# Kernel optimization log

Hardware: AMD Instinct MI355X
Metric: run time of the kernel (lower is better)

Reference implementation:

```python
import jax, jax.numpy as jnp
import numpy as np
import itertools

B, K, H, W = 64, 5, 320, 320
EPS = 1e-6
# All K! permutations (exact equivalent of scipy.linear_sum_assignment for KxK cost)
PERMS = np.array(list(itertools.permutations(range(K))), dtype=np.int32)  # [P, K]


def setup_inputs() -> dict:
    key = jax.random.key(0)
    k1, k2, k3 = jax.random.split(key, 3)
    return {
        "fg_logits": jax.random.normal(k1, (B, 1, H, W), dtype=jnp.float32),
        "slot_logits": jax.random.normal(k2, (B, K, H, W), dtype=jnp.float32),
        "target": jax.random.uniform(k3, (B, 1, H, W), dtype=jnp.float32),
    }


def reference(fg_logits, slot_logits, target):
    fg = target[:, 0]            # [B,H,W]
    bg = 1.0 - fg                # [B,H,W]
    # targets_b: index 0 = FG mask, 1..K-1 = BG mask (duplicated)  -> [B,K,H,W]
    targets = jnp.concatenate([fg[:, None], jnp.broadcast_to(bg[:, None], (B, K - 1, H, W))], axis=1)

    # IoU cost matrix on detached sigmoid probs (matches .detach())
    probs = jax.lax.stop_gradient(jax.nn.sigmoid(slot_logits))
    s = probs.reshape(B, K, -1)        # [B,K,N]
    t = targets.reshape(B, K, -1)      # [B,K,N]
    inter = jnp.einsum('bkn,bjn->bkj', s, t)           # [B,K,K]
    union = s.sum(-1)[:, :, None] + t.sum(-1)[:, None, :] - inter + EPS
    cost = 1.0 - inter / union                          # [B,K,K]

    # Exact Hungarian via brute force over K! permutations (K small)
    perms = jnp.asarray(PERMS)                          # [P,K]
    rows = jnp.arange(K)[None, :]                       # [1,K]
    perm_cost = cost[:, rows, perms].sum(-1)            # [B,P]
    best_perm = perms[jnp.argmin(perm_cost, axis=1)]    # [B,K] col_ind per sample

    # aligned[i] = targets[col_ind[i]]; targets[j] is fg iff j == 0
    is_fg = (best_perm == 0)[:, :, None, None]          # [B,K,1,1]
    aligned = jnp.where(is_fg, fg[:, None], bg[:, None])  # [B,K,H,W]

    # Stable sigmoid-BCE with logits, mean-reduced per sample then averaged over B
    x = slot_logits
    bce = jnp.maximum(x, 0.0) - x * aligned + jnp.log1p(jnp.exp(-jnp.abs(x)))
    return bce.mean()
```

## Files before the change

### kernel.cpp

```cpp
#include <hip/hip_runtime.h>


#define BB 64
#define KK 5
#define NPIX 102400
#define Q 50
#define SEG (NPIX / Q)
#define THREADS 256
#define ITERS (SEG / (THREADS * 4))
#define REC 32
#define NVAL 26
#define NBLK (BB * Q)

typedef float f4 __attribute__((ext_vector_type(4)));

__global__ void hung_pass1(const float* __restrict__ slot,
                           const float* __restrict__ tgt,
                           float* __restrict__ ws)
{
    const int bid = blockIdx.x;
    const int b   = bid / Q;
    const int q   = bid - b * Q;

    const float* sb = slot + (size_t)b * KK * NPIX + q * SEG;
    const float* t  = tgt  + (size_t)b * NPIX      + q * SEG;

    float aX[KK]  = {0,0,0,0,0};
    float aXF[KK] = {0,0,0,0,0};
    float aS[KK]  = {0,0,0,0,0};
    float aSF[KK] = {0,0,0,0,0};
    float aPX[KK] = {0,0,0,0,0};
    float Tf = 0.f;

    const int base = threadIdx.x * 4;
    #pragma unroll
    for (int i = 0; i < ITERS; ++i) {
        const int off = base + i * (THREADS * 4);
        const f4 fg4 = *reinterpret_cast<const f4*>(t + off);
        f4 x4[KK];
        #pragma unroll
        for (int k = 0; k < KK; ++k)
            x4[k] = *reinterpret_cast<const f4*>(sb + (size_t)k * NPIX + off);

        Tf += (fg4.x + fg4.y) + (fg4.z + fg4.w);

        #pragma unroll
        for (int k = 0; k < KK; ++k) {
            #pragma unroll
            for (int j = 0; j < 4; ++j) {
                const float x  = x4[k][j];
                const float fg = fg4[j];
                const float e  = __expf(-fabsf(x));
                const float L  = __logf(1.0f + e);
                const float d  = L + fmaxf(-x, 0.0f);
                const float s  = __expf(-d);
                aPX[k] += d;
                aX[k]  += x;
                aXF[k]  = fmaf(x, fg, aXF[k]);
                aS[k]  += s;
                aSF[k]  = fmaf(s, fg, aSF[k]);
            }
        }
    }

    float v[NVAL];
    #pragma unroll
    for (int k = 0; k < KK; ++k) {
        v[k*5+0] = aX[k];  v[k*5+1] = aXF[k]; v[k*5+2] = aS[k];
        v[k*5+3] = aSF[k]; v[k*5+4] = aPX[k];
    }
    v[25] = Tf;

    #pragma unroll
    for (int jv = 0; jv < NVAL; ++jv) {
        float x = v[jv];
        #pragma unroll
        for (int off = 32; off > 0; off >>= 1) x += __shfl_down(x, off, 64);
        v[jv] = x;
    }
    __shared__ float red[THREADS / 64][NVAL];
    const int lane = threadIdx.x & 63;
    const int w    = threadIdx.x >> 6;
    if (lane == 0) {
        #pragma unroll
        for (int jv = 0; jv < NVAL; ++jv) red[w][jv] = v[jv];
    }
    __syncthreads();
    if (threadIdx.x < NVAL) {
        const int jv = threadIdx.x;
        ws[(size_t)bid * REC + jv] =
            red[0][jv] + red[1][jv] + red[2][jv] + red[3][jv];
    }
}

__global__ __launch_bounds__(320) void hung_pass2(const float* __restrict__ ws,
                                                  float* __restrict__ out)
{
    __shared__ float red[BB][KK][6];
    const int t = threadIdx.x;
    {
        const int b = t / KK, k = t - (t / KK) * KK;
        float v[5] = {0, 0, 0, 0, 0};
        float tf = 0.f;
        for (int q = 0; q < Q; ++q) {
            const float* p = ws + (size_t)(b * Q + q) * REC;
            #pragma unroll
            for (int c = 0; c < 5; ++c) v[c] += p[k * 5 + c];
            if (k == 0) tf += p[25];
        }
        #pragma unroll
        for (int c = 0; c < 5; ++c) red[b][k][c] = v[c];
        if (k == 0) red[b][0][5] = tf;
    }
    __syncthreads();
    if (t < BB) {
        const int b = t;
        const float Tf = red[b][0][5];
        const float Tb = (float)NPIX - Tf;
        float best = 3.402823466e+38f; int kb = 0;
        float xfsum = 0.f, px = 0.f;
        #pragma unroll
        for (int k = 0; k < KK; ++k) {
            const float Sv = red[b][k][2], Iv = red[b][k][3];
            const float cf = 1.f - Iv / (Sv + Tf - Iv + 1e-6f);
            const float Ib = Sv - Iv;
            const float cb = 1.f - Ib / (Sv + Tb - Ib + 1e-6f);
            const float dd = cf - cb;
            if (dd < best) { best = dd; kb = k; }
            xfsum += red[b][k][1];
            px    += red[b][k][4];
        }
        float res = px + xfsum - (2.f * red[b][kb][1] - red[b][kb][0]);
        #pragma unroll
        for (int off = 32; off > 0; off >>= 1) res += __shfl_down(res, off, 64);
        if (b == 0) out[0] = res * (1.0f / 32768000.0f);
    }
}

extern "C" void kernel_launch(void* const* d_in, const int* in_sizes, int n_in,
                              void* d_out, int out_size, void* d_ws, size_t ws_size,
                              hipStream_t stream) {
    const float* slot = (const float*)d_in[1];
    const float* tgt  = (const float*)d_in[2];
    float* out = (float*)d_out;
    float* ws  = (float*)d_ws;

    hung_pass1<<<NBLK, THREADS, 0, stream>>>(slot, tgt, ws);
    hung_pass2<<<1, 320, 0, stream>>>(ws, out);
}
```

Baseline: 239.6 us.

## Double-buffer pass1 loads and cut segments per sample to enlarge work per block

Changes pass1 so each thread prefetches the next iteration's fg and slot vectors into a second register buffer before computing the current one, with a scheduling barrier to keep the loads ahead of the math. Q drops from 50 to 20, so there are fewer and longer blocks with 5 iterations each instead of 2. This aims to overlap global memory latency with the transcendental math and to reduce per-block reduction overhead. In exchange it raises register pressure, which may lower occupancy, and with fewer blocks the GPU may be less evenly filled.

Measured after the change: 236.0 us. About the same (-1.5%).

```diff
diff --git a/kernel.cpp b/kernel.cpp
--- a/kernel.cpp
+++ b/kernel.cpp
@@ -4,7 +4,7 @@
 #define BB 64
 #define KK 5
 #define NPIX 102400
-#define Q 50
+#define Q 20
 #define SEG (NPIX / Q)
 #define THREADS 256
 #define ITERS (SEG / (THREADS * 4))
@@ -13,6 +13,37 @@
 #define NBLK (BB * Q)
 
 typedef float f4 __attribute__((ext_vector_type(4)));
+
+#define LOADSEG(FGV, XV, OFF)                                              \
+    do {                                                                   \
+        const int _o = (OFF);                                              \
+        FGV = *reinterpret_cast<const f4*>(t + _o);                        \
+        _Pragma("unroll")                                                  \
+        for (int k = 0; k < KK; ++k)                                       \
+            XV[k] = *reinterpret_cast<const f4*>(sb + (size_t)k * NPIX + _o); \
+    } while (0)
+
+#define CONSUME(FGV, XV)                                                   \
+    do {                                                                   \
+        Tf += (FGV.x + FGV.y) + (FGV.z + FGV.w);                           \
+        _Pragma("unroll")                                                  \
+        for (int k = 0; k < KK; ++k) {                                     \
+            _Pragma("unroll")                                              \
+            for (int j = 0; j < 4; ++j) {                                  \
+                const float x  = XV[k][j];                                 \
+                const float fg = FGV[j];                                   \
+                const float e  = __expf(-fabsf(x));                        \
+                const float L  = __logf(1.0f + e);                         \
+                const float d  = L + fmaxf(-x, 0.0f);                      \
+                const float s  = __expf(-d);                               \
+                aPX[k] += d;                                               \
+                aX[k]  += x;                                               \
+                aXF[k]  = fmaf(x, fg, aXF[k]);                             \
+                aS[k]  += s;                                               \
+                aSF[k]  = fmaf(s, fg, aSF[k]);                             \
+            }                                                              \
+        }                                                                  \
+    } while (0)
 
 __global__ void hung_pass1(const float* __restrict__ slot,
                            const float* __restrict__ tgt,
@@ -33,34 +64,23 @@
     float Tf = 0.f;
 
     const int base = threadIdx.x * 4;
+
+    f4 Af, Bf;
+    f4 Ax[KK], Bx[KK];
+
+    LOADSEG(Af, Ax, base);
+
     #pragma unroll
     for (int i = 0; i < ITERS; ++i) {
-        const int off = base + i * (THREADS * 4);
-        const f4 fg4 = *reinterpret_cast<const f4*>(t + off);
-        f4 x4[KK];
-        #pragma unroll
-        for (int k = 0; k < KK; ++k)
-            x4[k] = *reinterpret_cast<const f4*>(sb + (size_t)k * NPIX + off);
-
-        Tf += (fg4.x + fg4.y) + (fg4.z + fg4.w);
-
-        #pragma unroll
-        for (int k = 0; k < KK; ++k) {
-            #pragma unroll
-            for (int j = 0; j < 4; ++j) {
-                const float x  = x4[k][j];
-                const float fg = fg4[j];
-                const float e  = __expf(-fabsf(x));
-                const float L  = __logf(1.0f + e);
-                const float d  = L + fmaxf(-x, 0.0f);
-                const float s  = __expf(-d);
-                aPX[k] += d;
-                aX[k]  += x;
-                aXF[k]  = fmaf(x, fg, aXF[k]);
-                aS[k]  += s;
-                aSF[k]  = fmaf(s, fg, aSF[k]);
-            }
+        const bool useA = ((i & 1) == 0);
+        if (i + 1 < ITERS) {
+            const int noff = base + (i + 1) * (THREADS * 4);
+            if (useA) LOADSEG(Bf, Bx, noff);
+            else      LOADSEG(Af, Ax, noff);
         }
+        __builtin_amdgcn_sched_barrier(0);
+        if (useA) CONSUME(Af, Ax);
+        else      CONSUME(Bf, Bx);
     }
 
     float v[NVAL];
```

## Split final reduction across per-sample blocks and use smaller pass-1 blocks

Applied to the files above, without the earlier changes.

Pass 1 now uses 128-thread blocks over 100 segments per sample, doubling the block count while keeping the same work per thread. The single-block second pass, whose threads each walked Q records serially, becomes one block per sample that reduces its records in parallel and picks the assignment, followed by a tiny 64-thread kernel for the final sum. This targets the serial tail of the old one-block reduction and gives the main pass finer load balance across CUs. In exchange it adds an extra kernel launch and doubles the workspace records.

Measured after the change: 227.9 us. 4.9% less time.

```diff
diff --git a/kernel.cpp b/kernel.cpp
--- a/kernel.cpp
+++ b/kernel.cpp
@@ -4,9 +4,9 @@
 #define BB 64
 #define KK 5
 #define NPIX 102400
-#define Q 50
+#define Q 100
 #define SEG (NPIX / Q)
-#define THREADS 256
+#define THREADS 128
 #define ITERS (SEG / (THREADS * 4))
 #define REC 32
 #define NVAL 26
@@ -14,9 +14,10 @@
 
 typedef float f4 __attribute__((ext_vector_type(4)));
 
-__global__ void hung_pass1(const float* __restrict__ slot,
-                           const float* __restrict__ tgt,
-                           float* __restrict__ ws)
+__global__ __launch_bounds__(THREADS)
+void hung_pass1(const float* __restrict__ slot,
+                const float* __restrict__ tgt,
+                float* __restrict__ ws)
 {
     const int bid = blockIdx.x;
     const int b   = bid / Q;
@@ -78,7 +79,7 @@
         for (int off = 32; off > 0; off >>= 1) x += __shfl_down(x, off, 64);
         v[jv] = x;
     }
-    __shared__ float red[THREADS / 64][NVAL];
+    __shared__ float red[2][NVAL];
     const int lane = threadIdx.x & 63;
     const int w    = threadIdx.x >> 6;
     if (lane == 0) {
@@ -88,53 +89,58 @@
     __syncthreads();
     if (threadIdx.x < NVAL) {
         const int jv = threadIdx.x;
-        ws[(size_t)bid * REC + jv] =
-            red[0][jv] + red[1][jv] + red[2][jv] + red[3][jv];
+        ws[(size_t)bid * REC + jv] = red[0][jv] + red[1][jv];
     }
 }
 
-__global__ __launch_bounds__(320) void hung_pass2(const float* __restrict__ ws,
-                                                  float* __restrict__ out)
+__global__ __launch_bounds__(128)
+void hung_pass2a(const float* __restrict__ ws,
+                 float* __restrict__ partial)
 {
-    __shared__ float red[BB][KK][6];
-    const int t = threadIdx.x;
-    {
-        const int b = t / KK, k = t - (t / KK) * KK;
-        float v[5] = {0, 0, 0, 0, 0};
-        float tf = 0.f;
-        for (int q = 0; q < Q; ++q) {
-            const float* p = ws + (size_t)(b * Q + q) * REC;
-            #pragma unroll
-            for (int c = 0; c < 5; ++c) v[c] += p[k * 5 + c];
-            if (k == 0) tf += p[25];
-        }
-        #pragma unroll
-        for (int c = 0; c < 5; ++c) red[b][k][c] = v[c];
-        if (k == 0) red[b][0][5] = tf;
+    __shared__ float r2[4][NVAL];
+    __shared__ float st[NVAL];
+    const int b = blockIdx.x;
+    const int c = threadIdx.x & 31;
+    const int g = threadIdx.x >> 5;
+    if (c < NVAL) {
+        float acc = 0.f;
+        const float* base = ws + (size_t)b * Q * REC;
+        for (int q = g; q < Q; q += 4)
+            acc += base[(size_t)q * REC + c];
+        r2[g][c] = acc;
     }
     __syncthreads();
-    if (t < BB) {
-        const int b = t;
-        const float Tf = red[b][0][5];
+    if (threadIdx.x < NVAL)
+        st[threadIdx.x] = (r2[0][threadIdx.x] + r2[1][threadIdx.x])
+                        + (r2[2][threadIdx.x] + r2[3][threadIdx.x]);
+    __syncthreads();
+    if (threadIdx.x == 0) {
+        const float Tf = st[25];
         const float Tb = (float)NPIX - Tf;
         float best = 3.402823466e+38f; int kb = 0;
         float xfsum = 0.f, px = 0.f;
         #pragma unroll
         for (int k = 0; k < KK; ++k) {
-            const float Sv = red[b][k][2], Iv = red[b][k][3];
+            const float Sv = st[k*5+2], Iv = st[k*5+3];
             const float cf = 1.f - Iv / (Sv + Tf - Iv + 1e-6f);
             const float Ib = Sv - Iv;
             const float cb = 1.f - Ib / (Sv + Tb - Ib + 1e-6f);
             const float dd = cf - cb;
             if (dd < best) { best = dd; kb = k; }
-            xfsum += red[b][k][1];
-            px    += red[b][k][4];
+            xfsum += st[k*5+1];
+            px    += st[k*5+4];
         }
-        float res = px + xfsum - (2.f * red[b][kb][1] - red[b][kb][0]);
-        #pragma unroll
-        for (int off = 32; off > 0; off >>= 1) res += __shfl_down(res, off, 64);
-        if (b == 0) out[0] = res * (1.0f / 32768000.0f);
+        partial[b] = px + xfsum - (2.f * st[kb*5+1] - st[kb*5+0]);
     }
+}
+
+__global__ __launch_bounds__(64)
+void hung_pass2b(const float* __restrict__ partial, float* __restrict__ out)
+{
+    float r = partial[threadIdx.x];
+    #pragma unroll
+    for (int off = 32; off > 0; off >>= 1) r += __shfl_down(r, off, 64);
+    if (threadIdx.x == 0) out[0] = r * (1.0f / 32768000.0f);
 }
 
 extern "C" void kernel_launch(void* const* d_in, const int* in_sizes, int n_in,
@@ -144,7 +150,9 @@
     const float* tgt  = (const float*)d_in[2];
     float* out = (float*)d_out;
     float* ws  = (float*)d_ws;
+    float* partial = ws + (size_t)NBLK * REC;
 
     hung_pass1<<<NBLK, THREADS, 0, stream>>>(slot, tgt, ws);
-    hung_pass2<<<1, 320, 0, stream>>>(ws, out);
+    hung_pass2a<<<BB, 128, 0, stream>>>(ws, partial);
+    hung_pass2b<<<1, 64, 0, stream>>>(partial, out);
 }
```

## Use persistent blocks with triple-buffered async global-to-LDS prefetch

Applied to the files above, without the earlier changes.

Cuts the grid from 50 segments per sample to 4, so there is roughly one block per CU. Each block walks 25 tiles of 1024 pixels and prefetches two tiles ahead with global_load_lds into a three-deep LDS ring, synchronising with vmcnt waits instead of barriers. The aim is to keep enough memory traffic in flight while shrinking the partial-result workspace and the pass-2 reduction. The cost is a single wave per SIMD with large LDS use, so latency hiding depends entirely on the manual pipeline depth and on in-wave ILP across the transcendental math.

Result: faster. 229.5 us (-4.2%).

```diff
diff --git a/kernel.cpp b/kernel.cpp
--- a/kernel.cpp
+++ b/kernel.cpp
@@ -4,13 +4,15 @@
 #define BB 64
 #define KK 5
 #define NPIX 102400
-#define Q 50
-#define SEG (NPIX / Q)
+#define QQ 4
+#define SEG (NPIX / QQ)
 #define THREADS 256
-#define ITERS (SEG / (THREADS * 4))
+#define TILE 1024
+#define TILES (SEG / TILE)
+#define NSTR 6
 #define REC 32
 #define NVAL 26
-#define NBLK (BB * Q)
+#define NBLK (BB * QQ)
 
 typedef float f4 __attribute__((ext_vector_type(4)));
 
@@ -18,12 +20,19 @@
                            const float* __restrict__ tgt,
                            float* __restrict__ ws)
 {
+    __shared__ __align__(16) float lds[3][NSTR][TILE];
+
     const int bid = blockIdx.x;
-    const int b   = bid / Q;
-    const int q   = bid - b * Q;
+    const int b   = bid >> 2;
+    const int q   = bid & 3;
+    const int tid = threadIdx.x;
+    const int wv  = tid >> 6;
 
-    const float* sb = slot + (size_t)b * KK * NPIX + q * SEG;
-    const float* t  = tgt  + (size_t)b * NPIX      + q * SEG;
+    const float* gs[NSTR];
+    #pragma unroll
+    for (int k = 0; k < KK; ++k)
+        gs[k] = slot + (size_t)(b * KK + k) * NPIX + (size_t)q * SEG;
+    gs[KK] = tgt + (size_t)b * NPIX + (size_t)q * SEG;
 
     float aX[KK]  = {0,0,0,0,0};
     float aXF[KK] = {0,0,0,0,0};
@@ -32,23 +41,40 @@
     float aPX[KK] = {0,0,0,0,0};
     float Tf = 0.f;
 
-    const int base = threadIdx.x * 4;
-    #pragma unroll
-    for (int i = 0; i < ITERS; ++i) {
-        const int off = base + i * (THREADS * 4);
-        const f4 fg4 = *reinterpret_cast<const f4*>(t + off);
-        f4 x4[KK];
-        #pragma unroll
-        for (int k = 0; k < KK; ++k)
-            x4[k] = *reinterpret_cast<const f4*>(sb + (size_t)k * NPIX + off);
+#define ISSUE(T)                                                             \
+    do {                                                                     \
+        const int _t  = (T);                                                 \
+        const int _bf = _t % 3;                                              \
+        _Pragma("unroll")                                                    \
+        for (int s = 0; s < NSTR; ++s) {                                     \
+            const float* _gp = gs[s] + _t * TILE + tid * 4;                  \
+            __builtin_amdgcn_global_load_lds(                                \
+                (const __attribute__((address_space(1))) void*)_gp,          \
+                (__attribute__((address_space(3))) void*)&lds[_bf][s][wv*256],\
+                16, 0, 0);                                                   \
+        }                                                                    \
+    } while (0)
 
+    ISSUE(0);
+    ISSUE(1);
+
+    for (int t = 0; t < TILES; ++t) {
+        if (t < TILES - 1) asm volatile("s_waitcnt vmcnt(6)" ::: "memory");
+        else               asm volatile("s_waitcnt vmcnt(0)" ::: "memory");
+        __builtin_amdgcn_sched_barrier(0);
+        if (t + 2 < TILES) ISSUE(t + 2);
+
+        const int bf = t % 3;
+        const int o  = tid * 4;
+        const f4 fg4 = *reinterpret_cast<const f4*>(&lds[bf][KK][o]);
         Tf += (fg4.x + fg4.y) + (fg4.z + fg4.w);
 
         #pragma unroll
         for (int k = 0; k < KK; ++k) {
+            const f4 x4 = *reinterpret_cast<const f4*>(&lds[bf][k][o]);
             #pragma unroll
             for (int j = 0; j < 4; ++j) {
-                const float x  = x4[k][j];
+                const float x  = x4[j];
                 const float fg = fg4[j];
                 const float e  = __expf(-fabsf(x));
                 const float L  = __logf(1.0f + e);
@@ -62,6 +88,7 @@
             }
         }
     }
+#undef ISSUE
 
     float v[NVAL];
     #pragma unroll
@@ -80,10 +107,9 @@
     }
     __shared__ float red[THREADS / 64][NVAL];
     const int lane = threadIdx.x & 63;
-    const int w    = threadIdx.x >> 6;
     if (lane == 0) {
         #pragma unroll
-        for (int jv = 0; jv < NVAL; ++jv) red[w][jv] = v[jv];
+        for (int jv = 0; jv < NVAL; ++jv) red[wv][jv] = v[jv];
     }
     __syncthreads();
     if (threadIdx.x < NVAL) {
@@ -102,8 +128,8 @@
         const int b = t / KK, k = t - (t / KK) * KK;
         float v[5] = {0, 0, 0, 0, 0};
         float tf = 0.f;
-        for (int q = 0; q < Q; ++q) {
-            const float* p = ws + (size_t)(b * Q + q) * REC;
+        for (int q = 0; q < QQ; ++q) {
+            const float* p = ws + (size_t)(b * QQ + q) * REC;
             #pragma unroll
             for (int c = 0; c < 5; ++c) v[c] += p[k * 5 + c];
             if (k == 0) tf += p[25];
```
